# Kernel optimization log

Hardware: AMD Instinct MI355X
Metric: run time of the kernel (lower is better)

The kernel has to match this reference:

```python
import jax, jax.numpy as jnp
import numpy as np

B, S, D = 4, 1024, 1024
H, HD = 16, 64
MAXPOS = 1024  # max_position_embeddings


def setup_inputs() -> dict:
    key = jax.random.key(0)
    ks = jax.random.split(key, 10)
    sc = 0.02
    return {
        "hidden_states": jax.random.normal(ks[0], (B, S, D), dtype=jnp.float32),
        "attention_mask": jnp.zeros((B, 1, 1, S), dtype=jnp.float32),
        "across_attention_prior": jax.random.uniform(ks[1], (B, H, S, S), dtype=jnp.float32),
        "head_mask": jnp.ones((1, H, 1, 1), dtype=jnp.float32),
        "Wq": jax.random.normal(ks[2], (D, D), dtype=jnp.float32) * sc,
        "bq": jnp.zeros((D,), dtype=jnp.float32),
        "Wk": jax.random.normal(ks[3], (D, D), dtype=jnp.float32) * sc,
        "bk": jnp.zeros((D,), dtype=jnp.float32),
        "Wv": jax.random.normal(ks[4], (D, D), dtype=jnp.float32) * sc,
        "bv": jnp.zeros((D,), dtype=jnp.float32),
        "dist_emb": jax.random.normal(ks[5], (2 * MAXPOS - 1, HD), dtype=jnp.float32) * sc,
    }


def _heads(x):
    # [B,S,D] -> [B,H,S,HD]
    return x.reshape(B, S, H, HD).transpose(0, 2, 1, 3)


def reference(hidden_states, attention_mask, across_attention_prior, head_mask,
              Wq, bq, Wk, bk, Wv, bv, dist_emb):
    q = _heads(hidden_states @ Wq + bq)  # [B,H,S,HD]
    k = _heads(hidden_states @ Wk + bk)
    v = _heads(hidden_states @ Wv + bv)

    scores = jnp.einsum("bhld,bhrd->bhlr", q, k)

    # relative_key_query positional bias
    pos = jnp.arange(S)
    distance = pos[:, None] - pos[None, :]  # [S,S]
    pe = dist_emb[distance + MAXPOS - 1]  # [S,S,HD] (l, r, d)
    scores = scores + jnp.einsum("bhld,lrd->bhlr", q, pe)
    scores = scores + jnp.einsum("bhrd,lrd->bhlr", k, pe)

    scores = scores / jnp.sqrt(jnp.float32(HD))
    scores = scores + attention_mask  # additive mask, broadcast [B,1,1,S]

    probs = jax.nn.softmax(scores, axis=-1)
    probs = probs * across_attention_prior  # post-softmax multiplicative prior
    probs = probs * head_mask  # dropout prob = 0 (eval)

    ctx = jnp.einsum("bhlr,bhrd->bhld", probs, v)
    ctx = ctx.transpose(0, 2, 1, 3).reshape(B, S, D)
    return ctx
```

## Files before the change

kernel.cpp:

```cpp
#include <hip/hip_runtime.h>


typedef unsigned short u16;
typedef unsigned int   u32;
typedef __attribute__((ext_vector_type(8))) short bfx8;
typedef __attribute__((ext_vector_type(4))) float f32x4;

#define MFMA_BF16(a, b, c) __builtin_amdgcn_mfma_f32_16x16x32_bf16(a, b, c, 0, 0, 0)

__device__ __forceinline__ u16 f2bf(float f) {
    union { float f; u32 u; } c; c.f = f;
    u32 u = c.u;
    return (u16)((u + 0x7FFFu + ((u >> 16) & 1u)) >> 16);
}
__device__ __forceinline__ float bf2f(u16 v) {
    union { u32 u; float f; } c; c.u = ((u32)v) << 16;
    return c.f;
}
__device__ __forceinline__ float load_f(const void* p, long i, bool bf) {
    return bf ? bf2f(((const u16*)p)[i]) : ((const float*)p)[i];
}
__device__ __forceinline__ u16 load_bf(const void* p, long i, bool bf) {
    return bf ? ((const u16*)p)[i] : f2bf(((const float*)p)[i]);
}

__device__ __forceinline__ void gload16(const u16* g, u16* l) {
    __builtin_amdgcn_global_load_lds(
        (__attribute__((address_space(1))) void*)g,
        (__attribute__((address_space(3))) void*)l, 16, 0, 0);
}

__global__ void k_detect(const u32* hid, int* flags) {
    __shared__ int cnt;
    if (threadIdx.x == 0) cnt = 0;
    __syncthreads();
    int c = 0;
    for (int i = threadIdx.x; i < 1024; i += 256) {
        u32 w = hid[i];
        u32 e = (w >> 7) & 0xFFu;
        if (e >= 100u && e <= 140u) c++;
    }
    atomicAdd(&cnt, c);
    __syncthreads();
    if (threadIdx.x == 0) flags[0] = (cnt > 512) ? 1 : 0;
}

__global__ void k_prep(const void* hidden, const void* dist, const void* mask,
                       const void* hm, const void* bq, const void* bk,
                       const void* bv, const int* flags, u16* hid_bf,
                       u16* dist_bf, float* mask_f, float* hm_f, float* bias_f) {
    const bool bf = flags[0] != 0;
    const long NH = 4L * 1024 * 1024, ND = 2047L * 64, NM = 4096, NB = 3072, NHM = 16;
    const long TOT = NH + ND + NM + NB + NHM;
    for (long i = (long)blockIdx.x * 256 + threadIdx.x; i < TOT;
         i += (long)gridDim.x * 256) {
        if (i < NH) hid_bf[i] = load_bf(hidden, i, bf);
        else if (i < NH + ND) dist_bf[i - NH] = load_bf(dist, i - NH, bf);
        else if (i < NH + ND + NM) mask_f[i - NH - ND] = load_f(mask, i - NH - ND, bf);
        else if (i < NH + ND + NM + NB) {
            long j = i - NH - ND - NM;
            const void* src = (j < 1024) ? bq : ((j < 2048) ? bk : bv);
            bias_f[j] = load_f(src, j & 1023, bf);
        } else {
            long j = i - NH - ND - NM - NB;
            hm_f[j] = load_f(hm, j, bf);
        }
    }
}

__global__ void k_transpose(const void* Wq, const void* Wk, const void* Wv,
                            const int* flags, u16* wt) {
    const bool bf = flags[0] != 0;
    __shared__ float t[32][33];
    const int z = blockIdx.z;
    const void* W = (z == 0) ? Wq : ((z == 1) ? Wk : Wv);
    int x = blockIdx.x * 32 + threadIdx.x;
    for (int i = 0; i < 4; i++) {
        int y = blockIdx.y * 32 + threadIdx.y + i * 8;
        t[threadIdx.y + i * 8][threadIdx.x] = load_f(W, (long)y * 1024 + x, bf);
    }
    __syncthreads();
    int x2 = blockIdx.y * 32 + threadIdx.x;
    u16* out = wt + (long)z * 1024 * 1024;
    for (int i = 0; i < 4; i++) {
        int y2 = blockIdx.x * 32 + threadIdx.y + i * 8;
        out[(long)y2 * 1024 + x2] = f2bf(t[threadIdx.x][threadIdx.y + i * 8]);
    }
}

__global__ __launch_bounds__(256, 2)
void k_qkv_gemm(const u16* A, const u16* Bt, const float* bias,
                u16* qb, u16* kb, u16* vb) {
    __shared__ u16 sA[128 * 32];
    __shared__ u16 sB[128 * 32];
    const int tid = threadIdx.x;
    const int w = tid >> 6, lane = tid & 63;
    const int quad = lane >> 4, nl = lane & 15;
    const int wr = w >> 1, wc = w & 1;
    const int n0 = blockIdx.x * 128, m0 = blockIdx.y * 128;

    f32x4 acc[4][4];
#pragma unroll
    for (int a = 0; a < 4; a++)
#pragma unroll
        for (int b = 0; b < 4; b++) acc[a][b] = (f32x4){0.f, 0.f, 0.f, 0.f};

    for (int kt = 0; kt < 32; kt++) {
        const int k0 = kt * 32;
        __syncthreads();
#pragma unroll
        for (int j = 0; j < 2; j++) {
            int row = 32 * w + 16 * j + (lane >> 2);
            int seg = lane & 3;
            gload16(A + (long)(m0 + row) * 1024 + k0 + seg * 8, sA + 1024 * w + 512 * j);
            gload16(Bt + (long)(n0 + row) * 1024 + k0 + seg * 8, sB + 1024 * w + 512 * j);
        }
        __syncthreads();

        bfx8 af[4], bfr[4];
#pragma unroll
        for (int f = 0; f < 4; f++) {
            af[f]  = *(const bfx8*)(sA + (64 * wr + 16 * f + nl) * 32 + quad * 8);
            bfr[f] = *(const bfx8*)(sB + (64 * wc + 16 * f + nl) * 32 + quad * 8);
        }
#pragma unroll
        for (int fm = 0; fm < 4; fm++)
#pragma unroll
            for (int fn = 0; fn < 4; fn++)
                acc[fm][fn] = MFMA_BF16(af[fm], bfr[fn], acc[fm][fn]);
    }

#pragma unroll
    for (int fm = 0; fm < 4; fm++) {
#pragma unroll
        for (int fn = 0; fn < 4; fn++) {
            int n = n0 + 64 * wc + 16 * fn + nl;
            int which = n >> 10, hcol = n & 1023;
            int h = hcol >> 6, hd = hcol & 63;
            u16* op = (which == 0) ? qb : ((which == 1) ? kb : vb);
            float bias_v = bias[n];
#pragma unroll
            for (int reg = 0; reg < 4; reg++) {
                int m = m0 + 64 * wr + 16 * fm + 4 * quad + reg;
                int b = m >> 10, s = m & 1023;
                float v = acc[fm][fn][reg] + bias_v;
                op[((long)((b * 16 + h) * 1024 + s)) * 64 + hd] = f2bf(v);
            }
        }
    }
}

__global__ __launch_bounds__(256, 2)
void k_attn(const u16* qb, const u16* kb, const u16* vb, const u16* Eb,
            const float* maskf, const float* hmf, const void* prior,
            const int* flags, void* out) {
    constexpr int PT = 72;
    constexpr int PD = 132;
    __shared__ __align__(16) char smem[79872];
    u16* sQ  = (u16*)(smem);
    u16* sK  = (u16*)(smem + 9216);
    u16* sVT = (u16*)(smem + 18432);
    u16* sE  = (u16*)(smem + 27648);
    u16* sDq = (u16*)(smem + 46080);
    u16* sDk = (u16*)(smem + 62976);
    u16* sP  = (u16*)(smem + 46080);

    const int tid = threadIdx.x;
    const int w = tid >> 6, lane = tid & 63;
    const int quad = lane >> 4, nl = lane & 15;
    const int bh = blockIdx.x, b = bh >> 4, h = bh & 15;
    const int l0 = blockIdx.y * 64;
    const bool bf = flags[0] != 0;

    const u16* qbh = qb + (long)bh * 65536;
    const u16* kbh = kb + (long)bh * 65536;
    const u16* vbh = vb + (long)bh * 65536;

#pragma unroll
    for (int p = 0; p < 2; p++) {
        int seg = tid + p * 256;
        int row = seg >> 3, s8 = seg & 7;
        *(int4*)(sQ + row * PT + s8 * 8) = *(const int4*)(qbh + (l0 + row) * 64 + s8 * 8);
    }

    f32x4 accv[4];
#pragma unroll
    for (int f = 0; f < 4; f++) accv[f] = (f32x4){0.f, 0.f, 0.f, 0.f};
    float zacc[4] = {0.f, 0.f, 0.f, 0.f};
    const int jb_base = l0 + 960;

    for (int it = 0; it < 16; it++) {
        const int r0 = it * 64;
        __syncthreads();
#pragma unroll
        for (int p = 0; p < 2; p++) {
            int seg = tid + p * 256;
            int row = seg >> 3, s8 = seg & 7;
            *(int4*)(sK + row * PT + s8 * 8) = *(const int4*)(kbh + (r0 + row) * 64 + s8 * 8);
        }
        const int jb = jb_base - r0;
#pragma unroll
        for (int p = 0; p < 4; p++) {
            int seg = tid + p * 256;
            int row = seg >> 3, s8 = seg & 7;
            int j = jb + row; if (j > 2046) j = 2046;
            *(int4*)(sE + row * PT + s8 * 8) = *(const int4*)(Eb + j * 64 + s8 * 8);
        }
        {
            int r = tid & 63, dg = (tid >> 6) * 8;
#pragma unroll
            for (int rep = 0; rep < 2; rep++) {
                int d0 = dg + rep * 32;
                int4 vv = *(const int4*)(vbh + (r0 + r) * 64 + d0);
                const u16* pv8 = (const u16*)&vv;
#pragma unroll
                for (int j2 = 0; j2 < 8; j2++) sVT[(d0 + j2) * PT + r] = pv8[j2];
            }
        }
        float pr[4][4], mval[4];
#pragma unroll
        for (int fn = 0; fn < 4; fn++) {
            mval[fn] = maskf[b * 1024 + r0 + fn * 16 + nl];
#pragma unroll
            for (int reg = 0; reg < 4; reg++) {
                long pidx = ((long)(bh * 1024 + l0 + 16 * w + 4 * quad + reg)) * 1024
                            + r0 + fn * 16 + nl;
                pr[fn][reg] = bf ? bf2f(((const u16*)prior)[pidx])
                                 : ((const float*)prior)[pidx];
            }
        }
        __syncthreads();

        bfx8 aq0 = *(const bfx8*)(sQ + (16 * w + nl) * PT + quad * 8);
        bfx8 aq1 = *(const bfx8*)(sQ + (16 * w + nl) * PT + quad * 8 + 32);
        bfx8 ak0 = *(const bfx8*)(sK + (16 * w + nl) * PT + quad * 8);
        bfx8 ak1 = *(const bfx8*)(sK + (16 * w + nl) * PT + quad * 8 + 32);

#pragma unroll
        for (int fc = 0; fc < 8; fc++) {
            bfx8 be0 = *(const bfx8*)(sE + (fc * 16 + nl) * PT + quad * 8);
            bfx8 be1 = *(const bfx8*)(sE + (fc * 16 + nl) * PT + quad * 8 + 32);
            f32x4 dq = (f32x4){0.f, 0.f, 0.f, 0.f};
            dq = MFMA_BF16(aq0, be0, dq);
            dq = MFMA_BF16(aq1, be1, dq);
            f32x4 dk = (f32x4){0.f, 0.f, 0.f, 0.f};
            dk = MFMA_BF16(ak0, be0, dk);
            dk = MFMA_BF16(ak1, be1, dk);
#pragma unroll
            for (int reg = 0; reg < 4; reg++) {
                int rr = 16 * w + 4 * quad + reg;
                sDq[rr * PD + fc * 16 + nl] = f2bf(dq[reg]);
                sDk[rr * PD + fc * 16 + nl] = f2bf(dk[reg]);
            }
        }
        f32x4 accs[4];
#pragma unroll
        for (int fn = 0; fn < 4; fn++) {
            bfx8 bk0 = *(const bfx8*)(sK + (fn * 16 + nl) * PT + quad * 8);
            bfx8 bk1 = *(const bfx8*)(sK + (fn * 16 + nl) * PT + quad * 8 + 32);
            f32x4 s = (f32x4){0.f, 0.f, 0.f, 0.f};
            s = MFMA_BF16(aq0, bk0, s);
            s = MFMA_BF16(aq1, bk1, s);
            accs[fn] = s;
        }
        __syncthreads();

        float pw[4][4];
#pragma unroll
        for (int fn = 0; fn < 4; fn++) {
#pragma unroll
            for (int reg = 0; reg < 4; reg++) {
                int li = 16 * w + 4 * quad + reg;
                int ri = 16 * fn + nl;
                int u = li - ri + 63;
                float s = (accs[fn][reg] + bf2f(sDq[li * PD + u])
                           + bf2f(sDk[ri * PD + u])) * 0.125f + mval[fn];
                float e = __expf(s);
                zacc[reg] += e;
                pw[fn][reg] = e * pr[fn][reg];
            }
        }
        __syncthreads();

#pragma unroll
        for (int fn = 0; fn < 4; fn++)
#pragma unroll
            for (int reg = 0; reg < 4; reg++)
                sP[(16 * w + 4 * quad + reg) * PT + fn * 16 + nl] = f2bf(pw[fn][reg]);

        bfx8 ap0 = *(const bfx8*)(sP + (16 * w + nl) * PT + quad * 8);
        bfx8 ap1 = *(const bfx8*)(sP + (16 * w + nl) * PT + quad * 8 + 32);
#pragma unroll
        for (int fd = 0; fd < 4; fd++) {
            bfx8 bv0 = *(const bfx8*)(sVT + (fd * 16 + nl) * PT + quad * 8);
            bfx8 bv1 = *(const bfx8*)(sVT + (fd * 16 + nl) * PT + quad * 8 + 32);
            accv[fd] = MFMA_BF16(ap0, bv0, accv[fd]);
            accv[fd] = MFMA_BF16(ap1, bv1, accv[fd]);
        }
    }

#pragma unroll
    for (int reg = 0; reg < 4; reg++) {
        float z = zacc[reg];
        z += __shfl_xor(z, 1);
        z += __shfl_xor(z, 2);
        z += __shfl_xor(z, 4);
        z += __shfl_xor(z, 8);
        zacc[reg] = z;
    }
    const float hm = hmf[h];
#pragma unroll
    for (int fd = 0; fd < 4; fd++) {
#pragma unroll
        for (int reg = 0; reg < 4; reg++) {
            int l = l0 + 16 * w + 4 * quad + reg;
            int d = fd * 16 + nl;
            float val = accv[fd][reg] * hm / zacc[reg];
            long oidx = ((long)(b * 1024 + l)) * 1024 + h * 64 + d;
            if (bf) ((u16*)out)[oidx] = f2bf(val);
            else    ((float*)out)[oidx] = val;
        }
    }
}

extern "C" void kernel_launch(void* const* d_in, const int* in_sizes, int n_in,
                              void* d_out, int out_size, void* d_ws, size_t ws_size,
                              hipStream_t stream) {
    char* ws = (char*)d_ws;
    int*   flags   = (int*)ws;
    u16*   hid_bf  = (u16*)(ws + 256);
    u16*   wt_bf   = (u16*)(ws + 8388864);
    u16*   dist_bf = (u16*)(ws + 14680320);
    float* mask_f  = (float*)(ws + 14942464);
    float* bias_f  = (float*)(ws + 14958848);
    float* hm_f    = (float*)(ws + 14971136);
    u16*   q_bf    = (u16*)(ws + 14971392);
    u16*   k_bf    = (u16*)(ws + 23360000);
    u16*   v_bf    = (u16*)(ws + 31748608);

    k_detect<<<1, 256, 0, stream>>>((const u32*)d_in[0], flags);
    k_prep<<<2048, 256, 0, stream>>>(d_in[0], d_in[10], d_in[1], d_in[3],
                                     d_in[5], d_in[7], d_in[9], flags,
                                     hid_bf, dist_bf, mask_f, hm_f, bias_f);
    k_transpose<<<dim3(32, 32, 3), dim3(32, 8), 0, stream>>>(
        d_in[4], d_in[6], d_in[8], flags, wt_bf);
    k_qkv_gemm<<<dim3(24, 32), 256, 0, stream>>>(hid_bf, wt_bf, bias_f,
                                                 q_bf, k_bf, v_bf);
    k_attn<<<dim3(64, 16), 256, 0, stream>>>(q_bf, k_bf, v_bf, dist_bf,
                                             mask_f, hm_f, d_in[2], flags, d_out);
}
```

Measured before the change: 515.9 us.

## Skip unused relative-position MFMA tiles, shrink LDS, direct-to-LDS swizzled loads

The attention kernel now computes only the positional-bias MFMA tiles each wave needs along the diagonal band and scatters them straight into compact per-(l,r) score buffers. This replaces the full 64x128 Dq/Dk buffers. Shared memory drops from about 78 KB to 50 KB so three blocks fit per CU, and launch bounds are raised to match. K and E tiles are loaded with direct global-to-LDS loads into XOR-swizzled layouts, and Q is held in registers. One barrier is removed by writing P in place over E. The added branches and scattered conditional stores could lead to divergence, and the higher occupancy target may increase register pressure.

Measured after the change: 588.3 us. 1.14x slower.

```diff
diff --git a/kernel.cpp b/kernel.cpp
--- a/kernel.cpp
+++ b/kernel.cpp
@@ -150,20 +150,19 @@
     }
 }
 
-__global__ __launch_bounds__(256, 2)
+__global__ __launch_bounds__(256, 3)
 void k_attn(const u16* qb, const u16* kb, const u16* vb, const u16* Eb,
             const float* maskf, const float* hmf, const void* prior,
             const int* flags, void* out) {
     constexpr int PT = 72;
-    constexpr int PD = 132;
-    __shared__ __align__(16) char smem[79872];
-    u16* sQ  = (u16*)(smem);
-    u16* sK  = (u16*)(smem + 9216);
-    u16* sVT = (u16*)(smem + 18432);
-    u16* sE  = (u16*)(smem + 27648);
-    u16* sDq = (u16*)(smem + 46080);
-    u16* sDk = (u16*)(smem + 62976);
-    u16* sP  = (u16*)(smem + 46080);
+    constexpr int PS = 68;
+    __shared__ __align__(16) char smem[51200];
+    u16* sE  = (u16*)(smem);
+    u16* sP  = (u16*)(smem);
+    u16* sK  = (u16*)(smem + 16384);
+    u16* sVT = (u16*)(smem + 24576);
+    u16* sSq = (u16*)(smem + 33792);
+    u16* sSk = (u16*)(smem + 42496);
 
     const int tid = threadIdx.x;
     const int w = tid >> 6, lane = tid & 63;
@@ -176,45 +175,51 @@
     const u16* kbh = kb + (long)bh * 65536;
     const u16* vbh = vb + (long)bh * 65536;
 
-#pragma unroll
-    for (int p = 0; p < 2; p++) {
-        int seg = tid + p * 256;
-        int row = seg >> 3, s8 = seg & 7;
-        *(int4*)(sQ + row * PT + s8 * 8) = *(const int4*)(qbh + (l0 + row) * 64 + s8 * 8);
-    }
+#define TILE_FRAG(base, R, h) \
+    (*(const bfx8*)((base) + (R) * 64 + ((((h) * 4 + quad) ^ ((R) & 7)) * 8)))
+
+    const u16* qrow = qbh + (l0 + 16 * w + nl) * 64;
+    const bfx8 aq0 = *(const bfx8*)(qrow + quad * 8);
+    const bfx8 aq1 = *(const bfx8*)(qrow + quad * 8 + 32);
 
     f32x4 accv[4];
 #pragma unroll
     for (int f = 0; f < 4; f++) accv[f] = (f32x4){0.f, 0.f, 0.f, 0.f};
     float zacc[4] = {0.f, 0.f, 0.f, 0.f};
     const int jb_base = l0 + 960;
+    const int dqlo = w, dqhi = w + 4;
+    const int dklo = 3 - w, dkhi = 7 - w;
 
     for (int it = 0; it < 16; it++) {
         const int r0 = it * 64;
-        __syncthreads();
-#pragma unroll
-        for (int p = 0; p < 2; p++) {
-            int seg = tid + p * 256;
-            int row = seg >> 3, s8 = seg & 7;
-            *(int4*)(sK + row * PT + s8 * 8) = *(const int4*)(kbh + (r0 + row) * 64 + s8 * 8);
-        }
         const int jb = jb_base - r0;
-#pragma unroll
-        for (int p = 0; p < 4; p++) {
-            int seg = tid + p * 256;
-            int row = seg >> 3, s8 = seg & 7;
-            int j = jb + row; if (j > 2046) j = 2046;
-            *(int4*)(sE + row * PT + s8 * 8) = *(const int4*)(Eb + j * 64 + s8 * 8);
-        }
+        __syncthreads();
+
         {
-            int r = tid & 63, dg = (tid >> 6) * 8;
+            const int rl = w * 8 + (lane >> 3), u = lane & 7;
+#pragma unroll
+            for (int p = 0; p < 2; p++) {
+                int row = p * 32 + rl;
+                gload16(kbh + (r0 + row) * 64 + ((u ^ (row & 7)) * 8),
+                        sK + p * 2048 + w * 512);
+            }
+#pragma unroll
+            for (int p = 0; p < 4; p++) {
+                int row = p * 32 + rl;
+                int j = jb + row; if (j > 2046) j = 2046;
+                gload16(Eb + (long)j * 64 + ((u ^ (row & 7)) * 8),
+                        sE + p * 2048 + w * 512);
+            }
+        }
+        {
+            const int dg = w * 8;
 #pragma unroll
             for (int rep = 0; rep < 2; rep++) {
                 int d0 = dg + rep * 32;
-                int4 vv = *(const int4*)(vbh + (r0 + r) * 64 + d0);
+                int4 vv = *(const int4*)(vbh + (r0 + lane) * 64 + d0);
                 const u16* pv8 = (const u16*)&vv;
 #pragma unroll
-                for (int j2 = 0; j2 < 8; j2++) sVT[(d0 + j2) * PT + r] = pv8[j2];
+                for (int j2 = 0; j2 < 8; j2++) sVT[(d0 + j2) * PT + lane] = pv8[j2];
             }
         }
         float pr[4][4], mval[4];
@@ -231,33 +236,46 @@
         }
         __syncthreads();
 
-        bfx8 aq0 = *(const bfx8*)(sQ + (16 * w + nl) * PT + quad * 8);
-        bfx8 aq1 = *(const bfx8*)(sQ + (16 * w + nl) * PT + quad * 8 + 32);
-        bfx8 ak0 = *(const bfx8*)(sK + (16 * w + nl) * PT + quad * 8);
-        bfx8 ak1 = *(const bfx8*)(sK + (16 * w + nl) * PT + quad * 8 + 32);
+        const bfx8 ak0 = TILE_FRAG(sK, 16 * w + nl, 0);
+        const bfx8 ak1 = TILE_FRAG(sK, 16 * w + nl, 1);
 
 #pragma unroll
         for (int fc = 0; fc < 8; fc++) {
-            bfx8 be0 = *(const bfx8*)(sE + (fc * 16 + nl) * PT + quad * 8);
-            bfx8 be1 = *(const bfx8*)(sE + (fc * 16 + nl) * PT + quad * 8 + 32);
-            f32x4 dq = (f32x4){0.f, 0.f, 0.f, 0.f};
-            dq = MFMA_BF16(aq0, be0, dq);
-            dq = MFMA_BF16(aq1, be1, dq);
-            f32x4 dk = (f32x4){0.f, 0.f, 0.f, 0.f};
-            dk = MFMA_BF16(ak0, be0, dk);
-            dk = MFMA_BF16(ak1, be1, dk);
-#pragma unroll
-            for (int reg = 0; reg < 4; reg++) {
-                int rr = 16 * w + 4 * quad + reg;
-                sDq[rr * PD + fc * 16 + nl] = f2bf(dq[reg]);
-                sDk[rr * PD + fc * 16 + nl] = f2bf(dk[reg]);
+            const bool uq = (fc >= dqlo) && (fc <= dqhi);
+            const bool uk = (fc >= dklo) && (fc <= dkhi);
+            if (!(uq || uk)) continue;
+            const int R = fc * 16 + nl;
+            const bfx8 be0 = TILE_FRAG(sE, R, 0);
+            const bfx8 be1 = TILE_FRAG(sE, R, 1);
+            if (uq) {
+                f32x4 dq = (f32x4){0.f, 0.f, 0.f, 0.f};
+                dq = MFMA_BF16(aq0, be0, dq);
+                dq = MFMA_BF16(aq1, be1, dq);
+#pragma unroll
+                for (int reg = 0; reg < 4; reg++) {
+                    int li = 16 * w + 4 * quad + reg;
+                    int ri = li + 63 - R;
+                    if (ri >= 0 && ri < 64) sSq[li * PS + ri] = f2bf(dq[reg]);
+                }
+            }
+            if (uk) {
+                f32x4 dk = (f32x4){0.f, 0.f, 0.f, 0.f};
+                dk = MFMA_BF16(ak0, be0, dk);
+                dk = MFMA_BF16(ak1, be1, dk);
+#pragma unroll
+                for (int reg = 0; reg < 4; reg++) {
+                    int ri = 16 * w + 4 * quad + reg;
+                    int li = ri + R - 63;
+                    if (li >= 0 && li < 64) sSk[li * PS + ri] = f2bf(dk[reg]);
+                }
             }
         }
         f32x4 accs[4];
 #pragma unroll
         for (int fn = 0; fn < 4; fn++) {
-            bfx8 bk0 = *(const bfx8*)(sK + (fn * 16 + nl) * PT + quad * 8);
-            bfx8 bk1 = *(const bfx8*)(sK + (fn * 16 + nl) * PT + quad * 8 + 32);
+            const int R = fn * 16 + nl;
+            const bfx8 bk0 = TILE_FRAG(sK, R, 0);
+            const bfx8 bk1 = TILE_FRAG(sK, R, 1);
             f32x4 s = (f32x4){0.f, 0.f, 0.f, 0.f};
             s = MFMA_BF16(aq0, bk0, s);
             s = MFMA_BF16(aq1, bk1, s);
@@ -265,39 +283,30 @@
         }
         __syncthreads();
 
-        float pw[4][4];
 #pragma unroll
         for (int fn = 0; fn < 4; fn++) {
 #pragma unroll
             for (int reg = 0; reg < 4; reg++) {
                 int li = 16 * w + 4 * quad + reg;
-                int ri = 16 * fn + nl;
-                int u = li - ri + 63;
-                float s = (accs[fn][reg] + bf2f(sDq[li * PD + u])
-                           + bf2f(sDk[ri * PD + u])) * 0.125f + mval[fn];
+                int col = fn * 16 + nl;
+                float s = (accs[fn][reg] + bf2f(sSq[li * PS + col])
+                           + bf2f(sSk[li * PS + col])) * 0.125f + mval[fn];
                 float e = __expf(s);
                 zacc[reg] += e;
-                pw[fn][reg] = e * pr[fn][reg];
-            }
-        }
-        __syncthreads();
-
-#pragma unroll
-        for (int fn = 0; fn < 4; fn++)
-#pragma unroll
-            for (int reg = 0; reg < 4; reg++)
-                sP[(16 * w + 4 * quad + reg) * PT + fn * 16 + nl] = f2bf(pw[fn][reg]);
-
-        bfx8 ap0 = *(const bfx8*)(sP + (16 * w + nl) * PT + quad * 8);
-        bfx8 ap1 = *(const bfx8*)(sP + (16 * w + nl) * PT + quad * 8 + 32);
+                sP[li * PT + col] = f2bf(e * pr[fn][reg]);
+            }
+        }
+        const bfx8 ap0 = *(const bfx8*)(sP + (16 * w + nl) * PT + quad * 8);
+        const bfx8 ap1 = *(const bfx8*)(sP + (16 * w + nl) * PT + quad * 8 + 32);
 #pragma unroll
         for (int fd = 0; fd < 4; fd++) {
-            bfx8 bv0 = *(const bfx8*)(sVT + (fd * 16 + nl) * PT + quad * 8);
-            bfx8 bv1 = *(const bfx8*)(sVT + (fd * 16 + nl) * PT + quad * 8 + 32);
+            const bfx8 bv0 = *(const bfx8*)(sVT + (fd * 16 + nl) * PT + quad * 8);
+            const bfx8 bv1 = *(const bfx8*)(sVT + (fd * 16 + nl) * PT + quad * 8 + 32);
             accv[fd] = MFMA_BF16(ap0, bv0, accv[fd]);
             accv[fd] = MFMA_BF16(ap1, bv1, accv[fd]);
         }
     }
+#undef TILE_FRAG
 
 #pragma unroll
     for (int reg = 0; reg < 4; reg++) {
```

## Register-prefetch next K/E/V tiles and use LDS-only barriers in attention loop

Applied to the files above, without the earlier changes.

The loop now loads the next iteration's K, distance-embedding and V tiles from global memory into registers while the current tile is being computed, then stores them to LDS at the top of the next iteration. __syncthreads is replaced with a barrier that waits only on LDS counters (lgkmcnt), so outstanding global prefetch loads are not drained at each barrier. This aims to hide global load latency behind MFMA work, at the cost of more registers held live, which may reduce occupancy.

New measurement: 522.9 us. No clear change (+1.3%).

```diff
diff --git a/kernel.cpp b/kernel.cpp
--- a/kernel.cpp
+++ b/kernel.cpp
@@ -28,6 +28,12 @@
     __builtin_amdgcn_global_load_lds(
         (__attribute__((address_space(1))) void*)g,
         (__attribute__((address_space(3))) void*)l, 16, 0, 0);
+}
+
+__device__ __forceinline__ void wg_barrier() {
+    asm volatile("s_waitcnt lgkmcnt(0)" ::: "memory");
+    __builtin_amdgcn_s_barrier();
+    asm volatile("" ::: "memory");
 }
 
 __global__ void k_detect(const u32* hid, int* flags) {
@@ -183,40 +189,50 @@
         *(int4*)(sQ + row * PT + s8 * 8) = *(const int4*)(qbh + (l0 + row) * 64 + s8 * 8);
     }
 
+    const int erow = tid >> 3, es8 = tid & 7;
+    const int jb_base = l0 + 960;
+
+    int4 nK0, nK1, nE0, nE1, nE2, nE3, nV0, nV1;
+    {
+        nK0 = *(const int4*)(kbh + (0 + erow) * 64 + es8 * 8);
+        nK1 = *(const int4*)(kbh + (32 + erow) * 64 + es8 * 8);
+        int j0 = jb_base + erow;       if (j0 > 2046) j0 = 2046;
+        int j1 = jb_base + 32 + erow;  if (j1 > 2046) j1 = 2046;
+        int j2 = jb_base + 64 + erow;  if (j2 > 2046) j2 = 2046;
+        int j3 = jb_base + 96 + erow;  if (j3 > 2046) j3 = 2046;
+        nE0 = *(const int4*)(Eb + (long)j0 * 64 + es8 * 8);
+        nE1 = *(const int4*)(Eb + (long)j1 * 64 + es8 * 8);
+        nE2 = *(const int4*)(Eb + (long)j2 * 64 + es8 * 8);
+        nE3 = *(const int4*)(Eb + (long)j3 * 64 + es8 * 8);
+        nV0 = *(const int4*)(vbh + (0 + lane) * 64 + w * 8);
+        nV1 = *(const int4*)(vbh + (0 + lane) * 64 + w * 8 + 32);
+    }
+
     f32x4 accv[4];
 #pragma unroll
     for (int f = 0; f < 4; f++) accv[f] = (f32x4){0.f, 0.f, 0.f, 0.f};
     float zacc[4] = {0.f, 0.f, 0.f, 0.f};
-    const int jb_base = l0 + 960;
 
     for (int it = 0; it < 16; it++) {
         const int r0 = it * 64;
-        __syncthreads();
-#pragma unroll
-        for (int p = 0; p < 2; p++) {
-            int seg = tid + p * 256;
-            int row = seg >> 3, s8 = seg & 7;
-            *(int4*)(sK + row * PT + s8 * 8) = *(const int4*)(kbh + (r0 + row) * 64 + s8 * 8);
-        }
-        const int jb = jb_base - r0;
-#pragma unroll
-        for (int p = 0; p < 4; p++) {
-            int seg = tid + p * 256;
-            int row = seg >> 3, s8 = seg & 7;
-            int j = jb + row; if (j > 2046) j = 2046;
-            *(int4*)(sE + row * PT + s8 * 8) = *(const int4*)(Eb + j * 64 + s8 * 8);
-        }
+        wg_barrier();
+
+        *(int4*)(sK + erow * PT + es8 * 8)        = nK0;
+        *(int4*)(sK + (32 + erow) * PT + es8 * 8) = nK1;
+        *(int4*)(sE + erow * PT + es8 * 8)        = nE0;
+        *(int4*)(sE + (32 + erow) * PT + es8 * 8) = nE1;
+        *(int4*)(sE + (64 + erow) * PT + es8 * 8) = nE2;
+        *(int4*)(sE + (96 + erow) * PT + es8 * 8) = nE3;
         {
-            int r = tid & 63, dg = (tid >> 6) * 8;
-#pragma unroll
-            for (int rep = 0; rep < 2; rep++) {
-                int d0 = dg + rep * 32;
-                int4 vv = *(const int4*)(vbh + (r0 + r) * 64 + d0);
-                const u16* pv8 = (const u16*)&vv;
-#pragma unroll
-                for (int j2 = 0; j2 < 8; j2++) sVT[(d0 + j2) * PT + r] = pv8[j2];
-            }
-        }
+            const u16* pv0 = (const u16*)&nV0;
+            const u16* pv1 = (const u16*)&nV1;
+#pragma unroll
+            for (int j2 = 0; j2 < 8; j2++) {
+                sVT[(w * 8 + j2) * PT + lane]      = pv0[j2];
+                sVT[(w * 8 + 32 + j2) * PT + lane] = pv1[j2];
+            }
+        }
+
         float pr[4][4], mval[4];
 #pragma unroll
         for (int fn = 0; fn < 4; fn++) {
@@ -229,7 +245,24 @@
                                  : ((const float*)prior)[pidx];
             }
         }
-        __syncthreads();
+
+        if (it < 15) {
+            const int r0n = r0 + 64;
+            const int jbn = jb_base - r0n;
+            nK0 = *(const int4*)(kbh + (r0n + erow) * 64 + es8 * 8);
+            nK1 = *(const int4*)(kbh + (r0n + 32 + erow) * 64 + es8 * 8);
+            int j0 = jbn + erow;       if (j0 > 2046) j0 = 2046;
+            int j1 = jbn + 32 + erow;  if (j1 > 2046) j1 = 2046;
+            int j2 = jbn + 64 + erow;  if (j2 > 2046) j2 = 2046;
+            int j3 = jbn + 96 + erow;  if (j3 > 2046) j3 = 2046;
+            nE0 = *(const int4*)(Eb + (long)j0 * 64 + es8 * 8);
+            nE1 = *(const int4*)(Eb + (long)j1 * 64 + es8 * 8);
+            nE2 = *(const int4*)(Eb + (long)j2 * 64 + es8 * 8);
+            nE3 = *(const int4*)(Eb + (long)j3 * 64 + es8 * 8);
+            nV0 = *(const int4*)(vbh + (r0n + lane) * 64 + w * 8);
+            nV1 = *(const int4*)(vbh + (r0n + lane) * 64 + w * 8 + 32);
+        }
+        wg_barrier();
 
         bfx8 aq0 = *(const bfx8*)(sQ + (16 * w + nl) * PT + quad * 8);
         bfx8 aq1 = *(const bfx8*)(sQ + (16 * w + nl) * PT + quad * 8 + 32);
@@ -263,7 +296,7 @@
             s = MFMA_BF16(aq1, bk1, s);
             accs[fn] = s;
         }
-        __syncthreads();
+        wg_barrier();
 
         float pw[4][4];
 #pragma unroll
@@ -280,7 +313,7 @@
                 pw[fn][reg] = e * pr[fn][reg];
             }
         }
-        __syncthreads();
+        wg_barrier();
 
 #pragma unroll
         for (int fn = 0; fn < 4; fn++)
```
